# Optimization experiments

Measured on AMD Instinct MI355X. Metric: run time of the kernel, lower is better.

Reference implementation:

```python
import jax, jax.numpy as jnp
import numpy as np

EMBED_DIM = 512
NUM_HEADS = 8
HEAD_DIM = EMBED_DIM // NUM_HEADS


def setup_inputs() -> dict:
    key = jax.random.key(0)
    ks = jax.random.split(key, 6)
    B, S, D = 2, 4096, EMBED_DIM
    scale = 1.0 / np.sqrt(D)
    inputs = jax.random.normal(ks[0], (B, S, D), dtype=jnp.float32)
    Wq = jax.random.normal(ks[1], (D, D), dtype=jnp.float32) * scale
    Wk = jax.random.normal(ks[2], (D, D), dtype=jnp.float32) * scale
    Wv = jax.random.normal(ks[3], (D, D), dtype=jnp.float32) * scale
    Wo = jax.random.normal(ks[4], (D, D), dtype=jnp.float32) * scale
    zeros = jnp.zeros((D,), dtype=jnp.float32)
    return {"inputs": inputs, "Wq": Wq, "bq": zeros, "Wk": Wk, "bk": zeros,
            "Wv": Wv, "bv": zeros, "Wo": Wo, "bo": zeros}


def _split_heads(x, B, S):
    # [B,S,D] -> [B,H,S,hd]
    return x.reshape(B, S, NUM_HEADS, HEAD_DIM).transpose(0, 2, 1, 3)


def reference(inputs, Wq, bq, Wk, bk, Wv, bv, Wo, bo):
    B, S, D = inputs.shape
    q = _split_heads(inputs @ Wq + bq, B, S)
    k = _split_heads(inputs @ Wk + bk, B, S)
    v = _split_heads(inputs @ Wv + bv, B, S)
    scale = 1.0 / jnp.sqrt(jnp.asarray(HEAD_DIM, dtype=inputs.dtype))
    # full [B,H,S,S] score matrix, as in the original naive SDPA
    scores = jnp.einsum('bhqd,bhkd->bhqk', q, k) * scale
    weights = jax.nn.softmax(scores, axis=-1)
    attn = jnp.einsum('bhqk,bhkd->bhqd', weights, v)
    attn = attn.transpose(0, 2, 1, 3).reshape(B, S, D)
    return attn @ Wo + bo
```

## Files before the change

### kernel.cpp

```cpp
#include <hip/hip_runtime.h>
#include <hip/hip_bf16.h>
#include <stdint.h>


typedef __bf16 bf16x8 __attribute__((ext_vector_type(8)));
typedef float f32x4 __attribute__((ext_vector_type(4)));

using as1_void = __attribute__((address_space(1))) void;
using as3_void = __attribute__((address_space(3))) void;

__device__ __forceinline__ void gload16(const void* g, void* l) {
    __builtin_amdgcn_global_load_lds((const as1_void*)g, (as3_void*)l, 16, 0, 0);
}

__device__ __forceinline__ f32x4 mfma16(bf16x8 a, bf16x8 b, f32x4 c) {
    return __builtin_amdgcn_mfma_f32_16x16x32_bf16(a, b, c, 0, 0, 0);
}

__device__ __forceinline__ uint32_t pkbf(float a, float b) {
    union { __hip_bfloat16 h[2]; uint32_t u; } r;
    r.h[0] = __float2bfloat16(a);
    r.h[1] = __float2bfloat16(b);
    return r.u;
}

__global__ void cvt_all(const float* __restrict__ X, __hip_bfloat16* __restrict__ Xb,
                        const float* __restrict__ w0, const float* __restrict__ w1,
                        const float* __restrict__ w2, const float* __restrict__ w3,
                        __hip_bfloat16* __restrict__ o0, __hip_bfloat16* __restrict__ o1,
                        __hip_bfloat16* __restrict__ o2, __hip_bfloat16* __restrict__ o3) {
    __shared__ float t[32][33];
    const int bid = blockIdx.x, tid = threadIdx.x;
    if (bid < 1024) {
        const float* W; __hip_bfloat16* O;
        switch (bid >> 8) {
            case 0: W = w0; O = o0; break;
            case 1: W = w1; O = o1; break;
            case 2: W = w2; O = o2; break;
            default: W = w3; O = o3; break;
        }
        int rem = bid & 255;
        int n0 = (rem & 15) * 32, k0 = (rem >> 4) * 32;
        int tx = tid & 31, ty = tid >> 5;
        for (int j = 0; j < 4; ++j)
            t[ty + 8 * j][tx] = W[(size_t)(k0 + ty + 8 * j) * 512 + n0 + tx];
        __syncthreads();
        for (int j = 0; j < 4; ++j)
            O[(size_t)(n0 + ty + 8 * j) * 512 + k0 + tx] = __float2bfloat16(t[tx][ty + 8 * j]);
    } else {
        int i = ((bid - 1024) * 256 + tid) * 4;
        float4 v = *reinterpret_cast<const float4*>(X + i);
        uint2 u;
        u.x = pkbf(v.x, v.y);
        u.y = pkbf(v.z, v.w);
        *reinterpret_cast<uint2*>(Xb + i) = u;
    }
}

__global__ __launch_bounds__(256, 2) void gemm_qkv(
    const __hip_bfloat16* __restrict__ A, const __hip_bfloat16* __restrict__ Bt,
    const float* __restrict__ bq, const float* __restrict__ bk, const float* __restrict__ bv,
    __hip_bfloat16* __restrict__ Qb, __hip_bfloat16* __restrict__ Kb,
    __hip_bfloat16* __restrict__ Vtb, float qs)
{
    const int K = 512;
    __shared__ __hip_bfloat16 Abuf[128 * 32];
    __shared__ __hip_bfloat16 Bbuf[128 * 32];
    const int tid = threadIdx.x, w = tid >> 6, lane = tid & 63;
    const int col = lane & 15, quad = lane >> 4;
    const int wr = w >> 1, wc = w & 1;
    const int tileN = blockIdx.x * 128, tileM = blockIdx.y * 128;

    f32x4 acc[4][4] = {};

    for (int k0 = 0; k0 < K; k0 += 32) {
        for (int i = 0; i < 2; ++i) {
            int g = w * 2 + i;
            int chunk = g * 64 + lane;
            int row = chunk >> 2, c8 = chunk & 3;
            gload16(A + (size_t)(tileM + row) * K + k0 + c8 * 8, Abuf + g * 512);
            gload16(Bt + (size_t)(tileN + row) * K + k0 + c8 * 8, Bbuf + g * 512);
        }
        __syncthreads();
        bf16x8 af[4], bfr[4];
        for (int mt = 0; mt < 4; ++mt)
            af[mt] = *reinterpret_cast<const bf16x8*>(Abuf + (wr * 64 + mt * 16 + col) * 32 + quad * 8);
        for (int nt = 0; nt < 4; ++nt)
            bfr[nt] = *reinterpret_cast<const bf16x8*>(Bbuf + (wc * 64 + nt * 16 + col) * 32 + quad * 8);
        for (int mt = 0; mt < 4; ++mt)
            for (int nt = 0; nt < 4; ++nt)
                acc[mt][nt] = mfma16(af[mt], bfr[nt], acc[mt][nt]);
        __syncthreads();
    }

    const int seg = (tileN + wc * 64) >> 9;
    const float* bias = (seg == 0) ? bq : (seg == 1) ? bk : bv;
    const float scale = (seg == 0) ? qs : 1.0f;
    __hip_bfloat16* outp = (seg == 0) ? Qb : (seg == 1) ? Kb : Vtb;

    for (int mt = 0; mt < 4; ++mt) {
        for (int nt = 0; nt < 4; ++nt) {
            int n = tileN + wc * 64 + nt * 16 + col;
            int nn = n & 511, h = nn >> 6, d = nn & 63;
            float bn = bias[nn];
            for (int r = 0; r < 4; ++r) {
                int m = tileM + wr * 64 + mt * 16 + quad * 4 + r;
                int b = m >> 12, s = m & 4095;
                float v = (acc[mt][nt][r] + bn) * scale;
                size_t off;
                if (seg < 2) off = (((size_t)(b * 8 + h) * 4096 + s) << 6) + d;
                else         off = (((size_t)(b * 8 + h) * 64 + d) << 12) + s;
                outp[off] = __float2bfloat16(v);
            }
        }
    }
}

__global__ __launch_bounds__(256, 2) void gemm_out(
    const __hip_bfloat16* __restrict__ A, const __hip_bfloat16* __restrict__ Bt,
    const float* __restrict__ bias, float* __restrict__ out)
{
    const int N = 512, K = 512;
    __shared__ __hip_bfloat16 Abuf[128 * 32];
    __shared__ __hip_bfloat16 Bbuf[64 * 32];
    const int tid = threadIdx.x, w = tid >> 6, lane = tid & 63;
    const int col = lane & 15, quad = lane >> 4;
    const int tileN = blockIdx.x * 64, tileM = blockIdx.y * 128;

    f32x4 acc[2][4] = {};

    for (int k0 = 0; k0 < K; k0 += 32) {
        for (int i = 0; i < 2; ++i) {
            int g = w * 2 + i;
            int chunk = g * 64 + lane;
            int row = chunk >> 2, c8 = chunk & 3;
            gload16(A + (size_t)(tileM + row) * K + k0 + c8 * 8, Abuf + g * 512);
        }
        {
            int row = tid >> 2, c8 = tid & 3;
            gload16(Bt + (size_t)(tileN + row) * K + k0 + c8 * 8, Bbuf + tid * 8);
        }
        __syncthreads();
        bf16x8 af[2], bfr[4];
        for (int mt = 0; mt < 2; ++mt)
            af[mt] = *reinterpret_cast<const bf16x8*>(Abuf + (w * 32 + mt * 16 + col) * 32 + quad * 8);
        for (int nt = 0; nt < 4; ++nt)
            bfr[nt] = *reinterpret_cast<const bf16x8*>(Bbuf + (nt * 16 + col) * 32 + quad * 8);
        for (int mt = 0; mt < 2; ++mt)
            for (int nt = 0; nt < 4; ++nt)
                acc[mt][nt] = mfma16(af[mt], bfr[nt], acc[mt][nt]);
        __syncthreads();
    }

    for (int mt = 0; mt < 2; ++mt) {
        for (int nt = 0; nt < 4; ++nt) {
            int n = tileN + nt * 16 + col;
            float bn = bias[n];
            for (int r = 0; r < 4; ++r) {
                int m = tileM + w * 32 + mt * 16 + quad * 4 + r;
                out[(size_t)m * N + n] = acc[mt][nt][r] + bn;
            }
        }
    }
}

__global__ __launch_bounds__(256) void flash(
    const __hip_bfloat16* __restrict__ Q,
    const __hip_bfloat16* __restrict__ Kq,
    const __hip_bfloat16* __restrict__ Vt,
    __hip_bfloat16* __restrict__ attnb)
{
    __shared__ __hip_bfloat16 KT[2][4096];
    __shared__ __hip_bfloat16 VB[2][4096];
    __shared__ uint32_t TB[4][1024];

    const int bh = blockIdx.y, b = bh >> 3, h = bh & 7;
    const int tid = threadIdx.x, w = tid >> 6, lane = tid & 63;
    const int col = lane & 15, quad = lane >> 4;
    const int q0 = blockIdx.x * 128 + w * 32;
    const int c7 = col & 7;

    const __hip_bfloat16* Qh = Q + (size_t)bh * 4096 * 64;
    const __hip_bfloat16* Kh = Kq + (size_t)bh * 4096 * 64;
    const __hip_bfloat16* Vh = Vt + (size_t)bh * 64 * 4096;

    bf16x8 aq[2][2];
    for (int qh = 0; qh < 2; ++qh)
        for (int ks = 0; ks < 2; ++ks)
            aq[qh][ks] = *reinterpret_cast<const bf16x8*>(
                Qh + (size_t)(q0 + qh * 16 + col) * 64 + ks * 32 + quad * 8);

    const __hip_bfloat16* ksrc[2];
    const __hip_bfloat16* vsrc[2];
    int ldsoff[2];
    for (int i = 0; i < 2; ++i) {
        int c = i * 256 + tid;
        int row = c >> 3, s8 = (c & 7) ^ (row & 7);
        ksrc[i] = Kh + row * 64 + s8 * 8;
        vsrc[i] = Vh + (size_t)row * 4096 + s8 * 8;
        ldsoff[i] = (i * 256 + w * 64) * 8;
    }

    bf16x8 ones;
    for (int j = 0; j < 8; ++j) ones[j] = (__bf16)1.0f;

    f32x4 o[4][2] = {};
    f32x4 accl[2] = {};
    f32x4 sc[2][4][2];

    uint32_t* TBw = &TB[w][0];
    uint2* TBw2 = reinterpret_cast<uint2*>(TBw);

    gload16(ksrc[0], &KT[0][ldsoff[0]]);
    gload16(ksrc[1], &KT[0][ldsoff[1]]);
    gload16(vsrc[0], &VB[0][ldsoff[0]]);
    gload16(vsrc[1], &VB[0][ldsoff[1]]);
    gload16(ksrc[0] + 4096, &KT[1][ldsoff[0]]);
    gload16(ksrc[1] + 4096, &KT[1][ldsoff[1]]);
    __syncthreads();

    for (int kg = 0; kg < 4; ++kg)
        for (int qh = 0; qh < 2; ++qh)
            sc[0][kg][qh] = (f32x4){0.f, 0.f, 0.f, 0.f};
    for (int ks = 0; ks < 2; ++ks)
        for (int kg = 0; kg < 4; ++kg) {
            bf16x8 ak = *reinterpret_cast<const bf16x8*>(
                &KT[0][(kg * 16 + col) * 64 + (((ks * 4 + quad) ^ c7) << 3)]);
            for (int qh = 0; qh < 2; ++qh)
                sc[0][kg][qh] = mfma16(ak, aq[qh][ks], sc[0][kg][qh]);
        }
    __syncthreads();

#define FLASH_BODY(KT_, P_)                                                     \
    {                                                                           \
        const int kt_ = (KT_);                                                  \
        int kk = kt_ + 2; if (kk > 63) kk = 63;                                 \
        gload16(ksrc[0] + (size_t)kk * 4096, &KT[(P_)][ldsoff[0]]);             \
        gload16(ksrc[1] + (size_t)kk * 4096, &KT[(P_)][ldsoff[1]]);             \
        gload16(vsrc[0] + (size_t)(kt_ + 1) * 64, &VB[1 - (P_)][ldsoff[0]]);    \
        gload16(vsrc[1] + (size_t)(kt_ + 1) * 64, &VB[1 - (P_)][ldsoff[1]]);    \
        for (int kg = 0; kg < 4; ++kg)                                          \
            for (int qh = 0; qh < 2; ++qh) {                                    \
                f32x4 v = sc[(P_)][kg][qh];                                     \
                uint2 u;                                                        \
                u.x = pkbf(__builtin_amdgcn_exp2f(v[0]),                        \
                           __builtin_amdgcn_exp2f(v[1]));                       \
                u.y = pkbf(__builtin_amdgcn_exp2f(v[2]),                        \
                           __builtin_amdgcn_exp2f(v[3]));                       \
                TBw2[(qh * 16 + col) * 16 +                                     \
                     (((kg * 2 + (quad >> 1)) ^ c7) << 1) + (quad & 1)] = u;    \
            }                                                                   \
        for (int kg = 0; kg < 4; ++kg)                                          \
            for (int qh = 0; qh < 2; ++qh)                                      \
                sc[1 - (P_)][kg][qh] = (f32x4){0.f, 0.f, 0.f, 0.f};             \
        for (int ks = 0; ks < 2; ++ks)                                          \
            for (int kg = 0; kg < 4; ++kg) {                                    \
                bf16x8 ak = *reinterpret_cast<const bf16x8*>(                   \
                    &KT[1 - (P_)][(kg * 16 + col) * 64 +                        \
                                  (((ks * 4 + quad) ^ c7) << 3)]);              \
                for (int qh = 0; qh < 2; ++qh)                                  \
                    sc[1 - (P_)][kg][qh] =                                      \
                        mfma16(ak, aq[qh][ks], sc[1 - (P_)][kg][qh]);           \
            }                                                                   \
        bf16x8 bp[2][2];                                                        \
        for (int qh = 0; qh < 2; ++qh)                                          \
            for (int ks = 0; ks < 2; ++ks)                                      \
                bp[qh][ks] = *reinterpret_cast<const bf16x8*>(                  \
                    &TBw[(qh * 16 + col) * 32 + (((ks * 4 + quad) ^ c7) << 2)]);\
        for (int ks = 0; ks < 2; ++ks) {                                        \
            for (int dt = 0; dt < 4; ++dt) {                                    \
                bf16x8 av = *reinterpret_cast<const bf16x8*>(                   \
                    &VB[(P_)][(dt * 16 + col) * 64 +                            \
                              (((ks * 4 + quad) ^ c7) << 3)]);                  \
                for (int qh = 0; qh < 2; ++qh)                                  \
                    o[dt][qh] = mfma16(av, bp[qh][ks], o[dt][qh]);              \
            }                                                                   \
            accl[0] = mfma16(ones, bp[0][ks], accl[0]);                         \
            accl[1] = mfma16(ones, bp[1][ks], accl[1]);                         \
        }                                                                       \
        __syncthreads();                                                        \
    }

    FLASH_BODY(0, 0)
    for (int kth = 0; kth < 31; ++kth) {
        FLASH_BODY(2 * kth + 1, 1)
        FLASH_BODY(2 * kth + 2, 0)
    }
    {
        for (int kg = 0; kg < 4; ++kg)
            for (int qh = 0; qh < 2; ++qh) {
                f32x4 v = sc[1][kg][qh];
                uint2 u;
                u.x = pkbf(__builtin_amdgcn_exp2f(v[0]), __builtin_amdgcn_exp2f(v[1]));
                u.y = pkbf(__builtin_amdgcn_exp2f(v[2]), __builtin_amdgcn_exp2f(v[3]));
                TBw2[(qh * 16 + col) * 16 + (((kg * 2 + (quad >> 1)) ^ c7) << 1) + (quad & 1)] = u;
            }
        bf16x8 bp[2][2];
        for (int qh = 0; qh < 2; ++qh)
            for (int ks = 0; ks < 2; ++ks)
                bp[qh][ks] = *reinterpret_cast<const bf16x8*>(
                    &TBw[(qh * 16 + col) * 32 + (((ks * 4 + quad) ^ c7) << 2)]);
        for (int ks = 0; ks < 2; ++ks) {
            for (int dt = 0; dt < 4; ++dt) {
                bf16x8 av = *reinterpret_cast<const bf16x8*>(
                    &VB[1][(dt * 16 + col) * 64 + (((ks * 4 + quad) ^ c7) << 3)]);
                for (int qh = 0; qh < 2; ++qh)
                    o[dt][qh] = mfma16(av, bp[qh][ks], o[dt][qh]);
            }
            accl[0] = mfma16(ones, bp[0][ks], accl[0]);
            accl[1] = mfma16(ones, bp[1][ks], accl[1]);
        }
    }
#undef FLASH_BODY

    for (int qh = 0; qh < 2; ++qh) {
        float inv = 1.0f / accl[qh][0];
        int s = q0 + qh * 16 + col;
        __hip_bfloat16* dst = attnb + ((size_t)b * 4096 + s) * 512 + h * 64 + quad * 4;
        for (int dt = 0; dt < 4; ++dt) {
            uint2 u;
            u.x = pkbf(o[dt][qh][0] * inv, o[dt][qh][1] * inv);
            u.y = pkbf(o[dt][qh][2] * inv, o[dt][qh][3] * inv);
            *reinterpret_cast<uint2*>(dst + dt * 16) = u;
        }
    }
}

extern "C" void kernel_launch(void* const* d_in, const int* in_sizes, int n_in,
                              void* d_out, int out_size, void* d_ws, size_t ws_size,
                              hipStream_t stream) {
    const float* X  = (const float*)d_in[0];
    const float* Wq = (const float*)d_in[1];
    const float* bq = (const float*)d_in[2];
    const float* Wk = (const float*)d_in[3];
    const float* bk = (const float*)d_in[4];
    const float* Wv = (const float*)d_in[5];
    const float* bv = (const float*)d_in[6];
    const float* Wo = (const float*)d_in[7];
    const float* bo = (const float*)d_in[8];
    float* out = (float*)d_out;

    char* ws = (char*)d_ws;
    __hip_bfloat16* Xb  = (__hip_bfloat16*)(ws);
    __hip_bfloat16* Wqt = (__hip_bfloat16*)(ws + ((size_t)8 << 20));
    __hip_bfloat16* Wkt = Wqt + 512 * 512;
    __hip_bfloat16* Wvt = Wkt + 512 * 512;
    __hip_bfloat16* Wot = Wvt + 512 * 512;
    __hip_bfloat16* Qb  = (__hip_bfloat16*)(ws + ((size_t)10 << 20));
    __hip_bfloat16* Kb  = (__hip_bfloat16*)(ws + ((size_t)18 << 20));
    __hip_bfloat16* Vtb = (__hip_bfloat16*)(ws + ((size_t)26 << 20));
    __hip_bfloat16* Atb = (__hip_bfloat16*)(ws + ((size_t)34 << 20));

    cvt_all<<<5120, 256, 0, stream>>>(X, Xb, Wq, Wk, Wv, Wo, Wqt, Wkt, Wvt, Wot);

    const float qs = 0.125f * 1.4426950408889634f;
    gemm_qkv<<<dim3(12, 64), 256, 0, stream>>>(Xb, Wqt, bq, bk, bv, Qb, Kb, Vtb, qs);
    flash<<<dim3(32, 16), 256, 0, stream>>>(Qb, Kb, Vtb, Atb);
    gemm_out<<<dim3(8, 64), 256, 0, stream>>>(Atb, Wot, bo, out);
}
```

Measured before the change: 214.1 us.

## Split flash block into 8 waves of 16 query rows each

The flash attention block grows from 256 to 512 threads, and each wave now owns 16 query rows instead of 32. The same 128 query rows per block are covered, with fewer accumulators per thread and more waves per CU to hide latency. Each thread now issues one K/V async load per stage instead of two. In exchange, every K/V fragment read from LDS feeds only one MFMA instead of two, which doubles LDS read traffic per useful FLOP, and barrier synchronisation now spans 8 waves.

```diff
diff --git a/kernel.cpp b/kernel.cpp
--- a/kernel.cpp
+++ b/kernel.cpp
@@ -164,7 +164,7 @@
     }
 }
 
-__global__ __launch_bounds__(256) void flash(
+__global__ __launch_bounds__(512, 4) void flash(
     const __hip_bfloat16* __restrict__ Q,
     const __hip_bfloat16* __restrict__ Kq,
     const __hip_bfloat16* __restrict__ Vt,
@@ -172,62 +172,54 @@
 {
     __shared__ __hip_bfloat16 KT[2][4096];
     __shared__ __hip_bfloat16 VB[2][4096];
-    __shared__ uint32_t TB[4][1024];
+    __shared__ uint32_t TB[8][512];
 
     const int bh = blockIdx.y, b = bh >> 3, h = bh & 7;
     const int tid = threadIdx.x, w = tid >> 6, lane = tid & 63;
     const int col = lane & 15, quad = lane >> 4;
-    const int q0 = blockIdx.x * 128 + w * 32;
+    const int q0 = blockIdx.x * 128 + w * 16;
     const int c7 = col & 7;
 
     const __hip_bfloat16* Qh = Q + (size_t)bh * 4096 * 64;
     const __hip_bfloat16* Kh = Kq + (size_t)bh * 4096 * 64;
     const __hip_bfloat16* Vh = Vt + (size_t)bh * 64 * 4096;
 
-    bf16x8 aq[2][2];
-    for (int qh = 0; qh < 2; ++qh)
-        for (int ks = 0; ks < 2; ++ks)
-            aq[qh][ks] = *reinterpret_cast<const bf16x8*>(
-                Qh + (size_t)(q0 + qh * 16 + col) * 64 + ks * 32 + quad * 8);
-
-    const __hip_bfloat16* ksrc[2];
-    const __hip_bfloat16* vsrc[2];
-    int ldsoff[2];
-    for (int i = 0; i < 2; ++i) {
-        int c = i * 256 + tid;
-        int row = c >> 3, s8 = (c & 7) ^ (row & 7);
-        ksrc[i] = Kh + row * 64 + s8 * 8;
-        vsrc[i] = Vh + (size_t)row * 4096 + s8 * 8;
-        ldsoff[i] = (i * 256 + w * 64) * 8;
+    bf16x8 aq[2];
+    for (int ks = 0; ks < 2; ++ks)
+        aq[ks] = *reinterpret_cast<const bf16x8*>(
+            Qh + (size_t)(q0 + col) * 64 + ks * 32 + quad * 8);
+
+    const __hip_bfloat16* ksrc;
+    const __hip_bfloat16* vsrc;
+    int ldsoff;
+    {
+        int row = tid >> 3, s8 = (tid & 7) ^ (row & 7);
+        ksrc = Kh + row * 64 + s8 * 8;
+        vsrc = Vh + (size_t)row * 4096 + s8 * 8;
+        ldsoff = tid * 8;
     }
 
     bf16x8 ones;
     for (int j = 0; j < 8; ++j) ones[j] = (__bf16)1.0f;
 
-    f32x4 o[4][2] = {};
-    f32x4 accl[2] = {};
-    f32x4 sc[2][4][2];
+    f32x4 o[4] = {};
+    f32x4 accl = {};
+    f32x4 sc[2][4];
 
     uint32_t* TBw = &TB[w][0];
     uint2* TBw2 = reinterpret_cast<uint2*>(TBw);
 
-    gload16(ksrc[0], &KT[0][ldsoff[0]]);
-    gload16(ksrc[1], &KT[0][ldsoff[1]]);
-    gload16(vsrc[0], &VB[0][ldsoff[0]]);
-    gload16(vsrc[1], &VB[0][ldsoff[1]]);
-    gload16(ksrc[0] + 4096, &KT[1][ldsoff[0]]);
-    gload16(ksrc[1] + 4096, &KT[1][ldsoff[1]]);
+    gload16(ksrc, &KT[0][ldsoff]);
+    gload16(vsrc, &VB[0][ldsoff]);
+    gload16(ksrc + 4096, &KT[1][ldsoff]);
     __syncthreads();
 
-    for (int kg = 0; kg < 4; ++kg)
-        for (int qh = 0; qh < 2; ++qh)
-            sc[0][kg][qh] = (f32x4){0.f, 0.f, 0.f, 0.f};
+    for (int kg = 0; kg < 4; ++kg) sc[0][kg] = (f32x4){0.f, 0.f, 0.f, 0.f};
     for (int ks = 0; ks < 2; ++ks)
         for (int kg = 0; kg < 4; ++kg) {
             bf16x8 ak = *reinterpret_cast<const bf16x8*>(
                 &KT[0][(kg * 16 + col) * 64 + (((ks * 4 + quad) ^ c7) << 3)]);
-            for (int qh = 0; qh < 2; ++qh)
-                sc[0][kg][qh] = mfma16(ak, aq[qh][ks], sc[0][kg][qh]);
+            sc[0][kg] = mfma16(ak, aq[ks], sc[0][kg]);
         }
     __syncthreads();
 
@@ -235,48 +227,39 @@
     {                                                                           \
         const int kt_ = (KT_);                                                  \
         int kk = kt_ + 2; if (kk > 63) kk = 63;                                 \
-        gload16(ksrc[0] + (size_t)kk * 4096, &KT[(P_)][ldsoff[0]]);             \
-        gload16(ksrc[1] + (size_t)kk * 4096, &KT[(P_)][ldsoff[1]]);             \
-        gload16(vsrc[0] + (size_t)(kt_ + 1) * 64, &VB[1 - (P_)][ldsoff[0]]);    \
-        gload16(vsrc[1] + (size_t)(kt_ + 1) * 64, &VB[1 - (P_)][ldsoff[1]]);    \
+        gload16(ksrc + (size_t)kk * 4096, &KT[(P_)][ldsoff]);                   \
+        gload16(vsrc + (size_t)(kt_ + 1) * 64, &VB[1 - (P_)][ldsoff]);          \
+        for (int kg = 0; kg < 4; ++kg) {                                        \
+            f32x4 v = sc[(P_)][kg];                                             \
+            uint2 u;                                                            \
+            u.x = pkbf(__builtin_amdgcn_exp2f(v[0]),                            \
+                       __builtin_amdgcn_exp2f(v[1]));                           \
+            u.y = pkbf(__builtin_amdgcn_exp2f(v[2]),                            \
+                       __builtin_amdgcn_exp2f(v[3]));                           \
+            TBw2[col * 16 +                                                     \
+                 (((kg * 2 + (quad >> 1)) ^ c7) << 1) + (quad & 1)] = u;        \
+        }                                                                       \
         for (int kg = 0; kg < 4; ++kg)                                          \
-            for (int qh = 0; qh < 2; ++qh) {                                    \
-                f32x4 v = sc[(P_)][kg][qh];                                     \
-                uint2 u;                                                        \
-                u.x = pkbf(__builtin_amdgcn_exp2f(v[0]),                        \
-                           __builtin_amdgcn_exp2f(v[1]));                       \
-                u.y = pkbf(__builtin_amdgcn_exp2f(v[2]),                        \
-                           __builtin_amdgcn_exp2f(v[3]));                       \
-                TBw2[(qh * 16 + col) * 16 +                                     \
-                     (((kg * 2 + (quad >> 1)) ^ c7) << 1) + (quad & 1)] = u;    \
-            }                                                                   \
-        for (int kg = 0; kg < 4; ++kg)                                          \
-            for (int qh = 0; qh < 2; ++qh)                                      \
-                sc[1 - (P_)][kg][qh] = (f32x4){0.f, 0.f, 0.f, 0.f};             \
+            sc[1 - (P_)][kg] = (f32x4){0.f, 0.f, 0.f, 0.f};                     \
         for (int ks = 0; ks < 2; ++ks)                                          \
             for (int kg = 0; kg < 4; ++kg) {                                    \
                 bf16x8 ak = *reinterpret_cast<const bf16x8*>(                   \
                     &KT[1 - (P_)][(kg * 16 + col) * 64 +                        \
                                   (((ks * 4 + quad) ^ c7) << 3)]);              \
-                for (int qh = 0; qh < 2; ++qh)                                  \
-                    sc[1 - (P_)][kg][qh] =                                      \
-                        mfma16(ak, aq[qh][ks], sc[1 - (P_)][kg][qh]);           \
+                sc[1 - (P_)][kg] = mfma16(ak, aq[ks], sc[1 - (P_)][kg]);        \
             }                                                                   \
-        bf16x8 bp[2][2];                                                        \
-        for (int qh = 0; qh < 2; ++qh)                                          \
-            for (int ks = 0; ks < 2; ++ks)                                      \
-                bp[qh][ks] = *reinterpret_cast<const bf16x8*>(                  \
-                    &TBw[(qh * 16 + col) * 32 + (((ks * 4 + quad) ^ c7) << 2)]);\
+        bf16x8 bp[2];                                                           \
+        for (int ks = 0; ks < 2; ++ks)                                          \
+            bp[ks] = *reinterpret_cast<const bf16x8*>(                          \
+                &TBw[col * 32 + (((ks * 4 + quad) ^ c7) << 2)]);                \
         for (int ks = 0; ks < 2; ++ks) {                                        \
             for (int dt = 0; dt < 4; ++dt) {                                    \
                 bf16x8 av = *reinterpret_cast<const bf16x8*>(                   \
                     &VB[(P_)][(dt * 16 + col) * 64 +                            \
                               (((ks * 4 + quad) ^ c7) << 3)]);                  \
-                for (int qh = 0; qh < 2; ++qh)                                  \
-                    o[dt][qh] = mfma16(av, bp[qh][ks], o[dt][qh]);              \
+                o[dt] = mfma16(av, bp[ks], o[dt]);                              \
             }                                                                   \
-            accl[0] = mfma16(ones, bp[0][ks], accl[0]);                         \
-            accl[1] = mfma16(ones, bp[1][ks], accl[1]);                         \
+            accl = mfma16(ones, bp[ks], accl);                                  \
         }                                                                       \
         __syncthreads();                                                        \
     }
@@ -287,40 +270,36 @@
         FLASH_BODY(2 * kth + 2, 0)
     }
     {
-        for (int kg = 0; kg < 4; ++kg)
-            for (int qh = 0; qh < 2; ++qh) {
-                f32x4 v = sc[1][kg][qh];
-                uint2 u;
-                u.x = pkbf(__builtin_amdgcn_exp2f(v[0]), __builtin_amdgcn_exp2f(v[1]));
-                u.y = pkbf(__builtin_amdgcn_exp2f(v[2]), __builtin_amdgcn_exp2f(v[3]));
-                TBw2[(qh * 16 + col) * 16 + (((kg * 2 + (quad >> 1)) ^ c7) << 1) + (quad & 1)] = u;
-            }
-        bf16x8 bp[2][2];
-        for (int qh = 0; qh < 2; ++qh)
-            for (int ks = 0; ks < 2; ++ks)
-                bp[qh][ks] = *reinterpret_cast<const bf16x8*>(
-                    &TBw[(qh * 16 + col) * 32 + (((ks * 4 + quad) ^ c7) << 2)]);
+        for (int kg = 0; kg < 4; ++kg) {
+            f32x4 v = sc[1][kg];
+            uint2 u;
+            u.x = pkbf(__builtin_amdgcn_exp2f(v[0]), __builtin_amdgcn_exp2f(v[1]));
+            u.y = pkbf(__builtin_amdgcn_exp2f(v[2]), __builtin_amdgcn_exp2f(v[3]));
+            TBw2[col * 16 + (((kg * 2 + (quad >> 1)) ^ c7) << 1) + (quad & 1)] = u;
+        }
+        bf16x8 bp[2];
+        for (int ks = 0; ks < 2; ++ks)
+            bp[ks] = *reinterpret_cast<const bf16x8*>(
+                &TBw[col * 32 + (((ks * 4 + quad) ^ c7) << 2)]);
         for (int ks = 0; ks < 2; ++ks) {
             for (int dt = 0; dt < 4; ++dt) {
                 bf16x8 av = *reinterpret_cast<const bf16x8*>(
                     &VB[1][(dt * 16 + col) * 64 + (((ks * 4 + quad) ^ c7) << 3)]);
-                for (int qh = 0; qh < 2; ++qh)
-                    o[dt][qh] = mfma16(av, bp[qh][ks], o[dt][qh]);
+                o[dt] = mfma16(av, bp[ks], o[dt]);
             }
-            accl[0] = mfma16(ones, bp[0][ks], accl[0]);
-            accl[1] = mfma16(ones, bp[1][ks], accl[1]);
+            accl = mfma16(ones, bp[ks], accl);
         }
     }
 #undef FLASH_BODY
 
-    for (int qh = 0; qh < 2; ++qh) {
-        float inv = 1.0f / accl[qh][0];
-        int s = q0 + qh * 16 + col;
+    {
+        float inv = 1.0f / accl[0];
+        int s = q0 + col;
         __hip_bfloat16* dst = attnb + ((size_t)b * 4096 + s) * 512 + h * 64 + quad * 4;
         for (int dt = 0; dt < 4; ++dt) {
             uint2 u;
-            u.x = pkbf(o[dt][qh][0] * inv, o[dt][qh][1] * inv);
-            u.y = pkbf(o[dt][qh][2] * inv, o[dt][qh][3] * inv);
+            u.x = pkbf(o[dt][0] * inv, o[dt][1] * inv);
+            u.y = pkbf(o[dt][2] * inv, o[dt][3] * inv);
             *reinterpret_cast<uint2*>(dst + dt * 16) = u;
         }
     }
@@ -355,6 +334,6 @@
 
     const float qs = 0.125f * 1.4426950408889634f;
     gemm_qkv<<<dim3(12, 64), 256, 0, stream>>>(Xb, Wqt, bq, bk, bv, Qb, Kb, Vtb, qs);
-    flash<<<dim3(32, 16), 256, 0, stream>>>(Qb, Kb, Vtb, Atb);
+    flash<<<dim3(32, 16), 512, 0, stream>>>(Qb, Kb, Vtb, Atb);
     gemm_out<<<dim3(8, 64), 256, 0, stream>>>(Atb, Wot, bo, out);
 }
```

Result: slower. 218.6 us (+2.1%).

## Triple-buffer K/V tiles in flash kernel with partial vmcnt waits and setprio

Applied to the files above, without the earlier changes.

Moves the flash attention loop from double to triple buffering of K and V tiles in LDS, prefetching K three tiles and V two tiles ahead. The full __syncthreads is replaced by s_waitcnt vmcnt(4) plus s_barrier, so the most recent loads can stay in flight across the barrier. s_setprio is raised around the MFMA sections to favour matrix work across waves. The cost is more LDS per block, which may lower occupancy, and it depends on the vmcnt accounting being exact.

```diff
diff --git a/kernel.cpp b/kernel.cpp
--- a/kernel.cpp
+++ b/kernel.cpp
@@ -170,8 +170,8 @@
     const __hip_bfloat16* __restrict__ Vt,
     __hip_bfloat16* __restrict__ attnb)
 {
-    __shared__ __hip_bfloat16 KT[2][4096];
-    __shared__ __hip_bfloat16 VB[2][4096];
+    __shared__ __hip_bfloat16 KT[3][4096];
+    __shared__ __hip_bfloat16 VB[3][4096];
     __shared__ uint32_t TB[4][1024];
 
     const int bh = blockIdx.y, b = bh >> 3, h = bh & 7;
@@ -217,7 +217,11 @@
     gload16(vsrc[1], &VB[0][ldsoff[1]]);
     gload16(ksrc[0] + 4096, &KT[1][ldsoff[0]]);
     gload16(ksrc[1] + 4096, &KT[1][ldsoff[1]]);
-    __syncthreads();
+    gload16(vsrc[0] + 64, &VB[1][ldsoff[0]]);
+    gload16(vsrc[1] + 64, &VB[1][ldsoff[1]]);
+    gload16(ksrc[0] + 2 * 4096, &KT[2][ldsoff[0]]);
+    gload16(ksrc[1] + 2 * 4096, &KT[2][ldsoff[1]]);
+    asm volatile("s_waitcnt vmcnt(8)\n\ts_barrier" ::: "memory");
 
     for (int kg = 0; kg < 4; ++kg)
         for (int qh = 0; qh < 2; ++qh)
@@ -229,19 +233,20 @@
             for (int qh = 0; qh < 2; ++qh)
                 sc[0][kg][qh] = mfma16(ak, aq[qh][ks], sc[0][kg][qh]);
         }
-    __syncthreads();
-
-#define FLASH_BODY(KT_, P_)                                                     \
+    asm volatile("s_waitcnt vmcnt(4)\n\ts_barrier" ::: "memory");
+
+#define FLASH_BODY(T_, SP, KW, KR, VW, VR)                                      \
     {                                                                           \
-        const int kt_ = (KT_);                                                  \
-        int kk = kt_ + 2; if (kk > 63) kk = 63;                                 \
-        gload16(ksrc[0] + (size_t)kk * 4096, &KT[(P_)][ldsoff[0]]);             \
-        gload16(ksrc[1] + (size_t)kk * 4096, &KT[(P_)][ldsoff[1]]);             \
-        gload16(vsrc[0] + (size_t)(kt_ + 1) * 64, &VB[1 - (P_)][ldsoff[0]]);    \
-        gload16(vsrc[1] + (size_t)(kt_ + 1) * 64, &VB[1 - (P_)][ldsoff[1]]);    \
+        const int kt_ = (T_);                                                   \
+        int kk = kt_ + 3; if (kk > 63) kk = 63;                                 \
+        int vv = kt_ + 2; if (vv > 63) vv = 63;                                 \
+        gload16(ksrc[0] + (size_t)kk * 4096, &KT[KW][ldsoff[0]]);               \
+        gload16(ksrc[1] + (size_t)kk * 4096, &KT[KW][ldsoff[1]]);               \
+        gload16(vsrc[0] + (size_t)vv * 64, &VB[VW][ldsoff[0]]);                 \
+        gload16(vsrc[1] + (size_t)vv * 64, &VB[VW][ldsoff[1]]);                 \
         for (int kg = 0; kg < 4; ++kg)                                          \
             for (int qh = 0; qh < 2; ++qh) {                                    \
-                f32x4 v = sc[(P_)][kg][qh];                                     \
+                f32x4 v = sc[SP][kg][qh];                                       \
                 uint2 u;                                                        \
                 u.x = pkbf(__builtin_amdgcn_exp2f(v[0]),                        \
                            __builtin_amdgcn_exp2f(v[1]));                       \
@@ -252,40 +257,52 @@
             }                                                                   \
         for (int kg = 0; kg < 4; ++kg)                                          \
             for (int qh = 0; qh < 2; ++qh)                                      \
-                sc[1 - (P_)][kg][qh] = (f32x4){0.f, 0.f, 0.f, 0.f};             \
+                sc[1 - (SP)][kg][qh] = (f32x4){0.f, 0.f, 0.f, 0.f};             \
+        __builtin_amdgcn_s_setprio(1);                                          \
         for (int ks = 0; ks < 2; ++ks)                                          \
             for (int kg = 0; kg < 4; ++kg) {                                    \
                 bf16x8 ak = *reinterpret_cast<const bf16x8*>(                   \
-                    &KT[1 - (P_)][(kg * 16 + col) * 64 +                        \
-                                  (((ks * 4 + quad) ^ c7) << 3)]);              \
+                    &KT[KR][(kg * 16 + col) * 64 +                              \
+                            (((ks * 4 + quad) ^ c7) << 3)]);                    \
                 for (int qh = 0; qh < 2; ++qh)                                  \
-                    sc[1 - (P_)][kg][qh] =                                      \
-                        mfma16(ak, aq[qh][ks], sc[1 - (P_)][kg][qh]);           \
+                    sc[1 - (SP)][kg][qh] =                                      \
+                        mfma16(ak, aq[qh][ks], sc[1 - (SP)][kg][qh]);           \
             }                                                                   \
+        __builtin_amdgcn_s_setprio(0);                                          \
         bf16x8 bp[2][2];                                                        \
         for (int qh = 0; qh < 2; ++qh)                                          \
             for (int ks = 0; ks < 2; ++ks)                                      \
                 bp[qh][ks] = *reinterpret_cast<const bf16x8*>(                  \
                     &TBw[(qh * 16 + col) * 32 + (((ks * 4 + quad) ^ c7) << 2)]);\
+        __builtin_amdgcn_s_setprio(1);                                          \
         for (int ks = 0; ks < 2; ++ks) {                                        \
             for (int dt = 0; dt < 4; ++dt) {                                    \
                 bf16x8 av = *reinterpret_cast<const bf16x8*>(                   \
-                    &VB[(P_)][(dt * 16 + col) * 64 +                            \
-                              (((ks * 4 + quad) ^ c7) << 3)]);                  \
+                    &VB[VR][(dt * 16 + col) * 64 +                              \
+                            (((ks * 4 + quad) ^ c7) << 3)]);                    \
                 for (int qh = 0; qh < 2; ++qh)                                  \
                     o[dt][qh] = mfma16(av, bp[qh][ks], o[dt][qh]);              \
             }                                                                   \
             accl[0] = mfma16(ones, bp[0][ks], accl[0]);                         \
             accl[1] = mfma16(ones, bp[1][ks], accl[1]);                         \
         }                                                                       \
-        __syncthreads();                                                        \
-    }
-
-    FLASH_BODY(0, 0)
-    for (int kth = 0; kth < 31; ++kth) {
-        FLASH_BODY(2 * kth + 1, 1)
-        FLASH_BODY(2 * kth + 2, 0)
-    }
+        __builtin_amdgcn_s_setprio(0);                                          \
+        asm volatile("s_waitcnt vmcnt(4)\n\ts_barrier" ::: "memory");           \
+    }
+
+    for (int t6 = 0; t6 < 60; t6 += 6) {
+        FLASH_BODY(t6 + 0, 0, 0, 1, 2, 0)
+        FLASH_BODY(t6 + 1, 1, 1, 2, 0, 1)
+        FLASH_BODY(t6 + 2, 0, 2, 0, 1, 2)
+        FLASH_BODY(t6 + 3, 1, 0, 1, 2, 0)
+        FLASH_BODY(t6 + 4, 0, 1, 2, 0, 1)
+        FLASH_BODY(t6 + 5, 1, 2, 0, 1, 2)
+    }
+    FLASH_BODY(60, 0, 0, 1, 2, 0)
+    FLASH_BODY(61, 1, 1, 2, 0, 1)
+    FLASH_BODY(62, 0, 2, 0, 1, 2)
+#undef FLASH_BODY
+
     {
         for (int kg = 0; kg < 4; ++kg)
             for (int qh = 0; qh < 2; ++qh) {
@@ -303,7 +320,7 @@
         for (int ks = 0; ks < 2; ++ks) {
             for (int dt = 0; dt < 4; ++dt) {
                 bf16x8 av = *reinterpret_cast<const bf16x8*>(
-                    &VB[1][(dt * 16 + col) * 64 + (((ks * 4 + quad) ^ c7) << 3)]);
+                    &VB[0][(dt * 16 + col) * 64 + (((ks * 4 + quad) ^ c7) << 3)]);
                 for (int qh = 0; qh < 2; ++qh)
                     o[dt][qh] = mfma16(av, bp[qh][ks], o[dt][qh]);
             }
@@ -311,7 +328,6 @@
             accl[1] = mfma16(ones, bp[1][ks], accl[1]);
         }
     }
-#undef FLASH_BODY
 
     for (int qh = 0; qh < 2; ++qh) {
         float inv = 1.0f / accl[qh][0];
```

After: 213.2 us. No clear change (-0.4%).

## Switch flash attention to 32x32x16 MFMA with permlane32 swap instead of LDS

Applied to the files above, without the earlier changes.

Rewrites the flash attention inner loop around 32x32x16 bf16 MFMA tiles instead of 16x16x32. The exponentiated score tile is moved into the B-operand layout for the PV product with v_permlane32_swap register exchanges, so the per-wave LDS staging buffer and its write/read round trip go away. It also adds a minimum-blocks hint of 2 to launch bounds. The larger accumulator tiles raise register pressure, and the lane-exchange layout must exactly match the MFMA operand layout to stay correct.

```diff
diff --git a/kernel.cpp b/kernel.cpp
--- a/kernel.cpp
+++ b/kernel.cpp
@@ -5,6 +5,7 @@
 
 typedef __bf16 bf16x8 __attribute__((ext_vector_type(8)));
 typedef float f32x4 __attribute__((ext_vector_type(4)));
+typedef float f32x16 __attribute__((ext_vector_type(16)));
 
 using as1_void = __attribute__((address_space(1))) void;
 using as3_void = __attribute__((address_space(3))) void;
@@ -15,6 +16,10 @@
 
 __device__ __forceinline__ f32x4 mfma16(bf16x8 a, bf16x8 b, f32x4 c) {
     return __builtin_amdgcn_mfma_f32_16x16x32_bf16(a, b, c, 0, 0, 0);
+}
+
+__device__ __forceinline__ f32x16 mfma32(bf16x8 a, bf16x8 b, f32x16 c) {
+    return __builtin_amdgcn_mfma_f32_32x32x16_bf16(a, b, c, 0, 0, 0);
 }
 
 __device__ __forceinline__ uint32_t pkbf(float a, float b) {
@@ -22,6 +27,17 @@
     r.h[0] = __float2bfloat16(a);
     r.h[1] = __float2bfloat16(b);
     return r.u;
+}
+
+__device__ __forceinline__ void pl32swap(uint32_t& a, uint32_t& b) {
+#if __has_builtin(__builtin_amdgcn_permlane32_swap)
+    typedef unsigned int uint32x2_t __attribute__((ext_vector_type(2)));
+    uint32x2_t r = __builtin_amdgcn_permlane32_swap(a, b, false, false);
+    a = r[0];
+    b = r[1];
+#else
+    asm volatile("v_permlane32_swap_b32 %0, %1" : "+v"(a), "+v"(b));
+#endif
 }
 
 __global__ void cvt_all(const float* __restrict__ X, __hip_bfloat16* __restrict__ Xb,
@@ -164,7 +180,7 @@
     }
 }
 
-__global__ __launch_bounds__(256) void flash(
+__global__ __launch_bounds__(256, 2) void flash(
     const __hip_bfloat16* __restrict__ Q,
     const __hip_bfloat16* __restrict__ Kq,
     const __hip_bfloat16* __restrict__ Vt,
@@ -172,27 +188,26 @@
 {
     __shared__ __hip_bfloat16 KT[2][4096];
     __shared__ __hip_bfloat16 VB[2][4096];
-    __shared__ uint32_t TB[4][1024];
-
-    const int bh = blockIdx.y, b = bh >> 3, h = bh & 7;
+
+    const int bh = blockIdx.y, b = bh >> 3, hq = bh & 7;
     const int tid = threadIdx.x, w = tid >> 6, lane = tid & 63;
-    const int col = lane & 15, quad = lane >> 4;
+    const int l31 = lane & 31, hh = lane >> 5, l7 = lane & 7;
     const int q0 = blockIdx.x * 128 + w * 32;
-    const int c7 = col & 7;
 
     const __hip_bfloat16* Qh = Q + (size_t)bh * 4096 * 64;
     const __hip_bfloat16* Kh = Kq + (size_t)bh * 4096 * 64;
     const __hip_bfloat16* Vh = Vt + (size_t)bh * 64 * 4096;
 
-    bf16x8 aq[2][2];
-    for (int qh = 0; qh < 2; ++qh)
-        for (int ks = 0; ks < 2; ++ks)
-            aq[qh][ks] = *reinterpret_cast<const bf16x8*>(
-                Qh + (size_t)(q0 + qh * 16 + col) * 64 + ks * 32 + quad * 8);
+    bf16x8 aq[4];
+#pragma unroll
+    for (int dk = 0; dk < 4; ++dk)
+        aq[dk] = *reinterpret_cast<const bf16x8*>(
+            Qh + (size_t)(q0 + l31) * 64 + dk * 16 + hh * 8);
 
     const __hip_bfloat16* ksrc[2];
     const __hip_bfloat16* vsrc[2];
     int ldsoff[2];
+#pragma unroll
     for (int i = 0; i < 2; ++i) {
         int c = i * 256 + tid;
         int row = c >> 3, s8 = (c & 7) ^ (row & 7);
@@ -202,14 +217,13 @@
     }
 
     bf16x8 ones;
+#pragma unroll
     for (int j = 0; j < 8; ++j) ones[j] = (__bf16)1.0f;
 
-    f32x4 o[4][2] = {};
-    f32x4 accl[2] = {};
-    f32x4 sc[2][4][2];
-
-    uint32_t* TBw = &TB[w][0];
-    uint2* TBw2 = reinterpret_cast<uint2*>(TBw);
+    const f32x16 z16 = {};
+    f32x16 o[2] = {};
+    f32x16 lacc = {};
+    f32x16 sc[2][2];
 
     gload16(ksrc[0], &KT[0][ldsoff[0]]);
     gload16(ksrc[1], &KT[0][ldsoff[1]]);
@@ -219,65 +233,70 @@
     gload16(ksrc[1] + 4096, &KT[1][ldsoff[1]]);
     __syncthreads();
 
-    for (int kg = 0; kg < 4; ++kg)
-        for (int qh = 0; qh < 2; ++qh)
-            sc[0][kg][qh] = (f32x4){0.f, 0.f, 0.f, 0.f};
-    for (int ks = 0; ks < 2; ++ks)
-        for (int kg = 0; kg < 4; ++kg) {
-            bf16x8 ak = *reinterpret_cast<const bf16x8*>(
-                &KT[0][(kg * 16 + col) * 64 + (((ks * 4 + quad) ^ c7) << 3)]);
-            for (int qh = 0; qh < 2; ++qh)
-                sc[0][kg][qh] = mfma16(ak, aq[qh][ks], sc[0][kg][qh]);
-        }
+#define QK_STEP(KR_, SP2_)                                                      \
+    _Pragma("unroll")                                                           \
+    for (int kg = 0; kg < 2; ++kg) {                                            \
+        _Pragma("unroll")                                                       \
+        for (int dk = 0; dk < 4; ++dk) {                                        \
+            bf16x8 ak = *reinterpret_cast<const bf16x8*>(                       \
+                &KT[KR_][(kg * 32 + l31) * 64 + (((dk * 2 + hh) ^ l7) << 3)]);  \
+            sc[SP2_][kg] = (dk == 0) ? mfma32(ak, aq[0], z16)                   \
+                                     : mfma32(ak, aq[dk], sc[SP2_][kg]);        \
+        }                                                                       \
+    }
+
+#define SOFTMAX_EXCHANGE(SP_)                                                   \
+    uint32_t U[8][2];                                                           \
+    _Pragma("unroll")                                                           \
+    for (int kg = 0; kg < 2; ++kg) {                                            \
+        f32x16 v = sc[SP_][kg];                                                 \
+        _Pragma("unroll")                                                       \
+        for (int rr = 0; rr < 4; ++rr) {                                        \
+            U[kg * 4 + rr][0] = pkbf(__builtin_amdgcn_exp2f(v[rr * 4 + 0]),     \
+                                     __builtin_amdgcn_exp2f(v[rr * 4 + 1]));    \
+            U[kg * 4 + rr][1] = pkbf(__builtin_amdgcn_exp2f(v[rr * 4 + 2]),     \
+                                     __builtin_amdgcn_exp2f(v[rr * 4 + 3]));    \
+        }                                                                       \
+    }                                                                           \
+    bf16x8 bp[4];                                                               \
+    _Pragma("unroll")                                                           \
+    for (int kb = 0; kb < 4; ++kb) {                                            \
+        _Pragma("unroll")                                                       \
+        for (int t2 = 0; t2 < 2; ++t2)                                          \
+            pl32swap(U[2 * kb][t2], U[2 * kb + 1][t2]);                         \
+        union { uint32_t u[4]; bf16x8 v8; } cc;                                 \
+        cc.u[0] = U[2 * kb][0];     cc.u[1] = U[2 * kb][1];                     \
+        cc.u[2] = U[2 * kb + 1][0]; cc.u[3] = U[2 * kb + 1][1];                 \
+        bp[kb] = cc.v8;                                                         \
+    }
+
+#define PV_STEP(VR_)                                                            \
+    _Pragma("unroll")                                                           \
+    for (int dg = 0; dg < 2; ++dg) {                                            \
+        _Pragma("unroll")                                                       \
+        for (int kb = 0; kb < 4; ++kb) {                                        \
+            bf16x8 av = *reinterpret_cast<const bf16x8*>(                       \
+                &VB[VR_][(dg * 32 + l31) * 64 + (((kb * 2 + hh) ^ l7) << 3)]);  \
+            o[dg] = mfma32(av, bp[kb], o[dg]);                                  \
+        }                                                                       \
+    }                                                                           \
+    _Pragma("unroll")                                                           \
+    for (int kb = 0; kb < 4; ++kb) lacc = mfma32(ones, bp[kb], lacc);
+
+    QK_STEP(0, 0)
     __syncthreads();
 
-#define FLASH_BODY(KT_, P_)                                                     \
+#define FLASH_BODY(T_, P_)                                                      \
     {                                                                           \
-        const int kt_ = (KT_);                                                  \
+        const int kt_ = (T_);                                                   \
         int kk = kt_ + 2; if (kk > 63) kk = 63;                                 \
         gload16(ksrc[0] + (size_t)kk * 4096, &KT[(P_)][ldsoff[0]]);             \
         gload16(ksrc[1] + (size_t)kk * 4096, &KT[(P_)][ldsoff[1]]);             \
         gload16(vsrc[0] + (size_t)(kt_ + 1) * 64, &VB[1 - (P_)][ldsoff[0]]);    \
         gload16(vsrc[1] + (size_t)(kt_ + 1) * 64, &VB[1 - (P_)][ldsoff[1]]);    \
-        for (int kg = 0; kg < 4; ++kg)                                          \
-            for (int qh = 0; qh < 2; ++qh) {                                    \
-                f32x4 v = sc[(P_)][kg][qh];                                     \
-                uint2 u;                                                        \
-                u.x = pkbf(__builtin_amdgcn_exp2f(v[0]),                        \
-                           __builtin_amdgcn_exp2f(v[1]));                       \
-                u.y = pkbf(__builtin_amdgcn_exp2f(v[2]),                        \
-                           __builtin_amdgcn_exp2f(v[3]));                       \
-                TBw2[(qh * 16 + col) * 16 +                                     \
-                     (((kg * 2 + (quad >> 1)) ^ c7) << 1) + (quad & 1)] = u;    \
-            }                                                                   \
-        for (int kg = 0; kg < 4; ++kg)                                          \
-            for (int qh = 0; qh < 2; ++qh)                                      \
-                sc[1 - (P_)][kg][qh] = (f32x4){0.f, 0.f, 0.f, 0.f};             \
-        for (int ks = 0; ks < 2; ++ks)                                          \
-            for (int kg = 0; kg < 4; ++kg) {                                    \
-                bf16x8 ak = *reinterpret_cast<const bf16x8*>(                   \
-                    &KT[1 - (P_)][(kg * 16 + col) * 64 +                        \
-                                  (((ks * 4 + quad) ^ c7) << 3)]);              \
-                for (int qh = 0; qh < 2; ++qh)                                  \
-                    sc[1 - (P_)][kg][qh] =                                      \
-                        mfma16(ak, aq[qh][ks], sc[1 - (P_)][kg][qh]);           \
-            }                                                                   \
-        bf16x8 bp[2][2];                                                        \
-        for (int qh = 0; qh < 2; ++qh)                                          \
-            for (int ks = 0; ks < 2; ++ks)                                      \
-                bp[qh][ks] = *reinterpret_cast<const bf16x8*>(                  \
-                    &TBw[(qh * 16 + col) * 32 + (((ks * 4 + quad) ^ c7) << 2)]);\
-        for (int ks = 0; ks < 2; ++ks) {                                        \
-            for (int dt = 0; dt < 4; ++dt) {                                    \
-                bf16x8 av = *reinterpret_cast<const bf16x8*>(                   \
-                    &VB[(P_)][(dt * 16 + col) * 64 +                            \
-                              (((ks * 4 + quad) ^ c7) << 3)]);                  \
-                for (int qh = 0; qh < 2; ++qh)                                  \
-                    o[dt][qh] = mfma16(av, bp[qh][ks], o[dt][qh]);              \
-            }                                                                   \
-            accl[0] = mfma16(ones, bp[0][ks], accl[0]);                         \
-            accl[1] = mfma16(ones, bp[1][ks], accl[1]);                         \
-        }                                                                       \
+        SOFTMAX_EXCHANGE(P_)                                                    \
+        QK_STEP(1 - (P_), 1 - (P_))                                             \
+        PV_STEP(P_)                                                             \
         __syncthreads();                                                        \
     }
 
@@ -287,42 +306,27 @@
         FLASH_BODY(2 * kth + 2, 0)
     }
     {
-        for (int kg = 0; kg < 4; ++kg)
-            for (int qh = 0; qh < 2; ++qh) {
-                f32x4 v = sc[1][kg][qh];
+        SOFTMAX_EXCHANGE(1)
+        PV_STEP(1)
+    }
+#undef FLASH_BODY
+#undef PV_STEP
+#undef SOFTMAX_EXCHANGE
+#undef QK_STEP
+
+    {
+        float inv = 1.0f / lacc[0];
+        int s = q0 + l31;
+        __hip_bfloat16* dst = attnb + ((size_t)b * 4096 + s) * 512 + hq * 64;
+#pragma unroll
+        for (int dg = 0; dg < 2; ++dg)
+#pragma unroll
+            for (int rr = 0; rr < 4; ++rr) {
                 uint2 u;
-                u.x = pkbf(__builtin_amdgcn_exp2f(v[0]), __builtin_amdgcn_exp2f(v[1]));
-                u.y = pkbf(__builtin_amdgcn_exp2f(v[2]), __builtin_amdgcn_exp2f(v[3]));
-                TBw2[(qh * 16 + col) * 16 + (((kg * 2 + (quad >> 1)) ^ c7) << 1) + (quad & 1)] = u;
+                u.x = pkbf(o[dg][rr * 4 + 0] * inv, o[dg][rr * 4 + 1] * inv);
+                u.y = pkbf(o[dg][rr * 4 + 2] * inv, o[dg][rr * 4 + 3] * inv);
+                *reinterpret_cast<uint2*>(dst + dg * 32 + rr * 8 + hh * 4) = u;
             }
-        bf16x8 bp[2][2];
-        for (int qh = 0; qh < 2; ++qh)
-            for (int ks = 0; ks < 2; ++ks)
-                bp[qh][ks] = *reinterpret_cast<const bf16x8*>(
-                    &TBw[(qh * 16 + col) * 32 + (((ks * 4 + quad) ^ c7) << 2)]);
-        for (int ks = 0; ks < 2; ++ks) {
-            for (int dt = 0; dt < 4; ++dt) {
-                bf16x8 av = *reinterpret_cast<const bf16x8*>(
-                    &VB[1][(dt * 16 + col) * 64 + (((ks * 4 + quad) ^ c7) << 3)]);
-                for (int qh = 0; qh < 2; ++qh)
-                    o[dt][qh] = mfma16(av, bp[qh][ks], o[dt][qh]);
-            }
-            accl[0] = mfma16(ones, bp[0][ks], accl[0]);
-            accl[1] = mfma16(ones, bp[1][ks], accl[1]);
-        }
-    }
-#undef FLASH_BODY
-
-    for (int qh = 0; qh < 2; ++qh) {
-        float inv = 1.0f / accl[qh][0];
-        int s = q0 + qh * 16 + col;
-        __hip_bfloat16* dst = attnb + ((size_t)b * 4096 + s) * 512 + h * 64 + quad * 4;
-        for (int dt = 0; dt < 4; ++dt) {
-            uint2 u;
-            u.x = pkbf(o[dt][qh][0] * inv, o[dt][qh][1] * inv);
-            u.y = pkbf(o[dt][qh][2] * inv, o[dt][qh][3] * inv);
-            *reinterpret_cast<uint2*>(dst + dt * 16) = u;
-        }
     }
 }
 
```

New measurement: 209.6 us. 2.1% less time.
